# Optimization experiments

Measured on AMD Instinct MI355X. Metric: run time of the kernel, lower is better.

## Reference

```python
import jax, jax.numpy as jnp
import numpy as np

B, M, E, NPOS, F, NHEAD, NLAYERS, DFF = 32, 512, 512, 1024, 768, 8, 2, 2048
S = M + 1

def _pe(embed, pad):
    pos = np.arange(pad, dtype=np.float32)[:, None]
    i = np.arange(embed)[None, :]
    ang = pos / np.power(10000.0, (i // 2 * 2.0) / embed)
    pe = np.where(i % 2 == 0, np.sin(ang), np.cos(ang))
    return jnp.asarray(pe, jnp.float32)

PE = _pe(E, M)  # [M, E] sinusoidal table, matches pos_embedding()

def _ln(x, w, b, eps=1e-5):
    mu = x.mean(-1, keepdims=True)
    var = ((x - mu) ** 2).mean(-1, keepdims=True)
    return (x - mu) / jnp.sqrt(var + eps) * w + b

def _mha(x, wi, bi, wo, bo):
    # x: [L, N, E] where L is the attended axis (torch seq dim)
    L, N, Em = x.shape
    Dh = Em // NHEAD
    q, k, v = jnp.split(x @ wi.T + bi, 3, axis=-1)
    q = q.reshape(L, N, NHEAD, Dh) * np.float32(1.0 / np.sqrt(Dh))
    k = k.reshape(L, N, NHEAD, Dh)
    v = v.reshape(L, N, NHEAD, Dh)
    att = jax.nn.softmax(jnp.einsum('lnhd,mnhd->nhlm', q, k), axis=-1)
    o = jnp.einsum('nhlm,mnhd->lnhd', att, v).reshape(L, N, Em)
    return o @ wo.T + bo

def _encoder(x, enc):
    wi, bi, wo, bo, ln1w, ln1b, ln2w, ln2b, w1, b1, w2, b2 = enc
    for l in range(NLAYERS):  # post-norm TransformerEncoderLayer, ReLU, eval mode
        x = _ln(x + _mha(x, wi[l], bi[l], wo[l], bo[l]), ln1w[l], ln1b[l])
        h = jax.nn.relu(x @ w1[l].T + b1[l]) @ w2[l].T + b2[l]
        x = _ln(x + h, ln2w[l], ln2b[l])
    return x

def _forward(pos1, pos2, bert_feature, final_base, emb_table, enc, w_model, w_disc, b_disc):
    emb_table = emb_table.at[0].set(0.0)  # padding_idx=0
    embed = emb_table[pos2] + PE          # [B, M, E]
    starts, ends = pos1[..., 0], pos1[..., 1]
    # loop breaks at first span with end==0: valid = prefix of nonzero ends
    valid = jnp.cumprod((ends != 0).astype(jnp.int32), axis=1).astype(bool)
    k = jnp.arange(M)
    cover = valid[:, :, None] & (starts[:, :, None] <= k) & (k < ends[:, :, None])  # [B, Mspan, Mpos]
    # later spans overwrite earlier ones -> take max covering span index
    span_id = jnp.max(jnp.where(cover, jnp.arange(M)[None, :, None], -1), axis=1)  # [B, Mpos]
    filled = jnp.take_along_axis(embed, jnp.clip(span_id, 0, M - 1)[..., None], axis=1)
    final = jnp.where(span_id[..., None] >= 0, filled, final_base)  # [B, M, E]
    cls = jnp.broadcast_to(emb_table[1], (B, 1, E))
    x = jnp.concatenate([cls, final], axis=1)  # [B, S, E]; torch encoder treats dim0 as seq
    x = _encoder(x, enc)
    pos_feature = jnp.tanh(x @ w_model.T)      # [B, S, F]
    z = jnp.concatenate([bert_feature, pos_feature], axis=-1) @ w_disc.T + b_disc
    return jax.nn.sigmoid(z)                   # [B, S, 1]

def setup_inputs():
    key = jax.random.key(0)
    ks = jax.random.split(key, 12)
    sc = 0.02
    n_valid, chunk = 120, 4  # contiguous spans [4j, 4j+4) for j < 120, then end==0 terminator
    j = np.arange(M)
    starts = np.where(j < n_valid, j * chunk, 0)
    ends = np.where(j < n_valid, j * chunk + chunk, 0)
    pos1 = np.broadcast_to(np.stack([starts, ends], -1), (B, M, 2)).astype(np.int32)
    return {
        'pos1': jnp.asarray(pos1),
        'pos2': jax.random.randint(ks[0], (B, M), 2, NPOS),
        'bert_feature': jax.random.normal(ks[1], (B, S, F), jnp.float32),
        'final_base': jax.random.uniform(ks[2], (B, M, E), jnp.float32),
        'emb_table': jax.random.normal(ks[3], (NPOS, E), jnp.float32) * sc,
        'enc_in_proj_w': jax.random.normal(ks[4], (NLAYERS, 3 * E, E), jnp.float32) * sc,
        'enc_in_proj_b': jnp.zeros((NLAYERS, 3 * E), jnp.float32),
        'enc_out_proj_w': jax.random.normal(ks[5], (NLAYERS, E, E), jnp.float32) * sc,
        'enc_out_proj_b': jnp.zeros((NLAYERS, E), jnp.float32),
        'enc_ln1_w': jnp.ones((NLAYERS, E), jnp.float32),
        'enc_ln1_b': jnp.zeros((NLAYERS, E), jnp.float32),
        'enc_ln2_w': jnp.ones((NLAYERS, E), jnp.float32),
        'enc_ln2_b': jnp.zeros((NLAYERS, E), jnp.float32),
        'enc_ffn_w1': jax.random.normal(ks[6], (NLAYERS, DFF, E), jnp.float32) * sc,
        'enc_ffn_b1': jnp.zeros((NLAYERS, DFF), jnp.float32),
        'enc_ffn_w2': jax.random.normal(ks[7], (NLAYERS, E, DFF), jnp.float32) * sc,
        'enc_ffn_b2': jnp.zeros((NLAYERS, E), jnp.float32),
        'w_model': jax.random.normal(ks[8], (F, E), jnp.float32) * sc,
        'w_disc': jax.random.normal(ks[9], (1, 2 * F), jnp.float32) * sc,
        'b_disc': jnp.zeros((1,), jnp.float32),
    }

def reference(pos1, pos2, bert_feature, final_base, emb_table,
              enc_in_proj_w, enc_in_proj_b, enc_out_proj_w, enc_out_proj_b,
              enc_ln1_w, enc_ln1_b, enc_ln2_w, enc_ln2_b,
              enc_ffn_w1, enc_ffn_b1, enc_ffn_w2, enc_ffn_b2,
              w_model, w_disc, b_disc):
    enc = (enc_in_proj_w, enc_in_proj_b, enc_out_proj_w, enc_out_proj_b,
           enc_ln1_w, enc_ln1_b, enc_ln2_w, enc_ln2_b,
           enc_ffn_w1, enc_ffn_b1, enc_ffn_w2, enc_ffn_b2)
    return _forward(pos1, pos2, bert_feature, final_base, emb_table, enc, w_model, w_disc, b_disc)
```

## Files before the change

### kernel.cpp

```cpp
#include <hip/hip_runtime.h>
#include <hip/hip_bf16.h>

#define B_   32
#define M_   512
#define E_   512
#define S_   513
#define T_   (B_ * S_)
#define TP_  16512
#define NH_  8
#define DH_  64
#define F_   768
#define DFF_ 2048

#define GMT_ 129

typedef short short8 __attribute__((ext_vector_type(8)));
typedef float floatx4 __attribute__((ext_vector_type(4)));

__device__ __forceinline__ float bf2f(unsigned short u) {
    return __uint_as_float(((unsigned int)u) << 16);
}
__device__ __forceinline__ unsigned short f2b_rne(float f) {
    unsigned int u = __float_as_uint(f);
    unsigned int r = u + 0x7FFF + ((u >> 16) & 1);
    return (unsigned short)(r >> 16);
}
__device__ __forceinline__ void gload16(const void* g, void* l) {
    __builtin_amdgcn_global_load_lds(
        (const __attribute__((address_space(1))) void*)g,
        (__attribute__((address_space(3))) void*)l, 16, 0, 0);
}
__device__ __forceinline__ void wait_vm0() { __builtin_amdgcn_s_waitcnt(0x0F70); }

__global__ void span_kernel(const int* __restrict__ pos1, int* __restrict__ span) {
    int b = blockIdx.x;
    __shared__ int st[M_], en[M_];
    __shared__ int nv;
    int tid = threadIdx.x;
    for (int j = tid; j < M_; j += 256) {
        st[j] = pos1[(b * M_ + j) * 2];
        en[j] = pos1[(b * M_ + j) * 2 + 1];
    }
    __syncthreads();
    if (tid == 0) {
        int n = M_;
        for (int j = 0; j < M_; ++j) if (en[j] == 0) { n = j; break; }
        nv = n;
    }
    __syncthreads();
    int n = nv;
    for (int k = tid; k < M_; k += 256) {
        int best = -1;
        for (int j = 0; j < n; ++j)
            if (st[j] <= k && k < en[j]) best = j;
        span[b * M_ + k] = best;
    }
}

__global__ void f2b5_kernel(const float* __restrict__ s0, const float* __restrict__ s1,
                            const float* __restrict__ s2, const float* __restrict__ s3,
                            const float* __restrict__ s4,
                            unsigned short* __restrict__ dst,
                            int c0, int c1, int c2, int c3, int c4) {
    int i = blockIdx.x * 256 + threadIdx.x;
    if (i >= c4) return;
    float v;
    if      (i < c0) v = s0[i];
    else if (i < c1) v = s1[i - c0];
    else if (i < c2) v = s2[i - c1];
    else if (i < c3) v = s3[i - c2];
    else             v = s4[i - c3];
    dst[i] = f2b_rne(v);
}

__global__ void build_x(const float* __restrict__ emb,
                        const int* __restrict__ pos2,
                        const float* __restrict__ fbase,
                        const int* __restrict__ span,
                        float* __restrict__ x,
                        unsigned short* __restrict__ xb) {
    long long idx = (long long)blockIdx.x * blockDim.x + threadIdx.x;
    if (idx >= (long long)T_ * E_) return;
    int e = (int)(idx % E_);
    int t = (int)(idx / E_);
    int s = t % S_;
    int b = t / S_;
    float val;
    if (s == 0) {
        val = emb[E_ + e];
    } else {
        int k = s - 1;
        int sid = span[b * M_ + k];
        if (sid >= 0) {
            int p = pos2[b * M_ + sid];
            float ex = (float)((e >> 1) << 1) * (1.0f / 512.0f);
            float ang = (float)sid * exp2f(-ex * 13.287712379549449f);
            float pe = (e & 1) ? cosf(ang) : sinf(ang);
            val = emb[(size_t)p * E_ + e] + pe;
        } else {
            val = fbase[((size_t)b * M_ + k) * E_ + e];
        }
    }
    x[idx] = val;
    xb[idx] = f2b_rne(val);
}

template <int ACT, int KT>
__global__ __launch_bounds__(256, 4) void gemm_bf16(const unsigned short* __restrict__ A,
                                                    const unsigned short* __restrict__ W,
                                                    const float* __restrict__ bias,
                                                    unsigned short* __restrict__ Cb,
                                                    int T, int O) {
    constexpr int K = KT;
    constexpr int NSTEP = K / 32;
    __shared__ __align__(16) unsigned short sA[2][128 * 32];
    __shared__ __align__(16) unsigned short sB[2][128 * 32];
    int tid = threadIdx.x;
    int lane = tid & 63, wv = tid >> 6;
    int wr = (wv >> 1) * 64, wc = (wv & 1) * 64;

    int gn = O / 128;
    int per_panel = 8 * gn;
    int id = blockIdx.x;
    int p = id / per_panel;
    int r = id - p * per_panel;
    int mrem = GMT_ - p * 8; if (mrem > 8) mrem = 8;
    int mt = p * 8 + r % mrem;
    int nt = r / mrem;
    int t0 = mt * 128, o0 = nt * 128;

    floatx4 acc[4][4] = {};

    const unsigned short* Ag = A + (size_t)(t0 + wv * 32 + (lane >> 2)) * K + (lane & 3) * 8;
    const unsigned short* Bg = W + (size_t)(o0 + wv * 32 + (lane >> 2)) * K + (lane & 3) * 8;
    const size_t row16 = (size_t)16 * K;
    unsigned short* dA0 = &sA[0][wv * 1024];
    unsigned short* dB0 = &sB[0][wv * 1024];

    int fr = lane & 15;
    int fk = (lane >> 4) * 8;

    gload16(Ag, dA0);
    gload16(Ag + row16, dA0 + 512);
    gload16(Bg, dB0);
    gload16(Bg + row16, dB0 + 512);
    wait_vm0();
    __syncthreads();

#pragma unroll 2
    for (int s = 0; s < NSTEP; ++s) {
        const int cur = s & 1;
        if (s + 1 < NSTEP) {
            const int k = (s + 1) * 32;
            unsigned short* dA = &sA[cur ^ 1][wv * 1024];
            unsigned short* dB = &sB[cur ^ 1][wv * 1024];
            gload16(Ag + k, dA);
            gload16(Ag + row16 + k, dA + 512);
            gload16(Bg + k, dB);
            gload16(Bg + row16 + k, dB + 512);
        }

        short8 af[4], bfr[4];
#pragma unroll
        for (int i = 0; i < 4; ++i)
            af[i] = *(const short8*)&sA[cur][(wr + i * 16 + fr) * 32 + fk];
#pragma unroll
        for (int j = 0; j < 4; ++j)
            bfr[j] = *(const short8*)&sB[cur][(wc + j * 16 + fr) * 32 + fk];
#pragma unroll
        for (int i = 0; i < 4; ++i)
#pragma unroll
            for (int j = 0; j < 4; ++j)
                acc[i][j] = __builtin_amdgcn_mfma_f32_16x16x32_bf16(af[i], bfr[j], acc[i][j], 0, 0, 0);

        wait_vm0();
        __syncthreads();
    }

    int cr = (lane >> 4) * 4;
    int cc = lane & 15;
#pragma unroll
    for (int i = 0; i < 4; ++i) {
#pragma unroll
        for (int j = 0; j < 4; ++j) {
            int gn_ = o0 + wc + j * 16 + cc;
            float bv = bias ? bias[gn_] : 0.f;
#pragma unroll
            for (int rr = 0; rr < 4; ++rr) {
                int gm_ = t0 + wr + i * 16 + cr + rr;
                if (gm_ >= T) continue;
                float v = acc[i][j][rr] + bv;
                if (ACT == 1) v = fmaxf(v, 0.f);
                if (ACT == 2) v = tanhf(v);
                Cb[(size_t)gm_ * O + gn_] = f2b_rne(v);
            }
        }
    }
}

__global__ __launch_bounds__(64) void attn_mfma(const unsigned short* __restrict__ qkv,
                                                unsigned short* __restrict__ o) {
    __shared__ __align__(16) unsigned short vt[64 * 40];
    __shared__ __align__(16) unsigned short ps[32 * 40];
    int s = blockIdx.x, h = blockIdx.y;
    int lane = threadIdx.x;
    int hd = h * 64;
    int fr = lane & 15, fq = lane >> 4;

    {
        int m = lane >> 1;
        int d0 = (lane & 1) * 32;
        const unsigned short* vrow = qkv + ((size_t)m * S_ + s) * 1536 + 1024 + hd + d0;
        short8 v0 = *(const short8*)(vrow);
        short8 v1 = *(const short8*)(vrow + 8);
        short8 v2 = *(const short8*)(vrow + 16);
        short8 v3 = *(const short8*)(vrow + 24);
#pragma unroll
        for (int j = 0; j < 8; ++j) {
            vt[(d0 + j) * 40 + m]      = (unsigned short)v0[j];
            vt[(d0 + 8 + j) * 40 + m]  = (unsigned short)v1[j];
            vt[(d0 + 16 + j) * 40 + m] = (unsigned short)v2[j];
            vt[(d0 + 24 + j) * 40 + m] = (unsigned short)v3[j];
        }
    }

    floatx4 c[2][2] = {};
#pragma unroll
    for (int ks = 0; ks < 2; ++ks) {
        short8 aq[2], bk[2];
#pragma unroll
        for (int lt = 0; lt < 2; ++lt) {
            int l = lt * 16 + fr;
            aq[lt] = *(const short8*)(qkv + ((size_t)l * S_ + s) * 1536 + hd + ks * 32 + fq * 8);
        }
#pragma unroll
        for (int mt = 0; mt < 2; ++mt) {
            int m = mt * 16 + fr;
            bk[mt] = *(const short8*)(qkv + ((size_t)m * S_ + s) * 1536 + 512 + hd + ks * 32 + fq * 8);
        }
#pragma unroll
        for (int lt = 0; lt < 2; ++lt)
#pragma unroll
            for (int mt = 0; mt < 2; ++mt)
                c[lt][mt] = __builtin_amdgcn_mfma_f32_16x16x32_bf16(aq[lt], bk[mt], c[lt][mt], 0, 0, 0);
    }

#pragma unroll
    for (int lt = 0; lt < 2; ++lt) {
#pragma unroll
        for (int r = 0; r < 4; ++r) {
            float a = c[lt][0][r] * 0.125f;
            float b = c[lt][1][r] * 0.125f;
            float mx = fmaxf(a, b);
#pragma unroll
            for (int off = 1; off < 16; off <<= 1) mx = fmaxf(mx, __shfl_xor(mx, off));
            float ea = expf(a - mx), eb = expf(b - mx);
            float sm = ea + eb;
#pragma unroll
            for (int off = 1; off < 16; off <<= 1) sm += __shfl_xor(sm, off);
            float inv = 1.f / sm;
            int l = lt * 16 + fq * 4 + r;
            ps[l * 40 + fr]      = f2b_rne(ea * inv);
            ps[l * 40 + 16 + fr] = f2b_rne(eb * inv);
        }
    }
    __syncthreads();

    short8 pa[2], vb[4];
#pragma unroll
    for (int lt = 0; lt < 2; ++lt)
        pa[lt] = *(const short8*)&ps[(lt * 16 + fr) * 40 + fq * 8];
#pragma unroll
    for (int dt = 0; dt < 4; ++dt)
        vb[dt] = *(const short8*)&vt[(dt * 16 + fr) * 40 + fq * 8];

    floatx4 oa[2][4] = {};
#pragma unroll
    for (int lt = 0; lt < 2; ++lt)
#pragma unroll
        for (int dt = 0; dt < 4; ++dt)
            oa[lt][dt] = __builtin_amdgcn_mfma_f32_16x16x32_bf16(pa[lt], vb[dt], oa[lt][dt], 0, 0, 0);

#pragma unroll
    for (int lt = 0; lt < 2; ++lt)
#pragma unroll
        for (int dt = 0; dt < 4; ++dt)
#pragma unroll
            for (int r = 0; r < 4; ++r) {
                int l = lt * 16 + fq * 4 + r;
                o[((size_t)l * S_ + s) * E_ + hd + dt * 16 + fr] = f2b_rne(oa[lt][dt][r]);
            }
}

__global__ __launch_bounds__(256) void add_ln(float* __restrict__ x,
                                              unsigned short* __restrict__ xb,
                                              const unsigned short* __restrict__ h,
                                              const float* __restrict__ w,
                                              const float* __restrict__ b) {
    int t = blockIdx.x;
    float* xr = x + (size_t)t * E_;
    const unsigned short* hr = h + (size_t)t * E_;
    int i0 = threadIdx.x * 2;
    float2 xv = *(const float2*)&xr[i0];
    ushort2 hv = *(const ushort2*)&hr[i0];
    float v0 = xv.x + bf2f(hv.x), v1 = xv.y + bf2f(hv.y);

    __shared__ float red[4];
    float sum = v0 + v1;
    for (int off = 32; off; off >>= 1) sum += __shfl_down(sum, off);
    if ((threadIdx.x & 63) == 0) red[threadIdx.x >> 6] = sum;
    __syncthreads();
    float mu = (red[0] + red[1] + red[2] + red[3]) * (1.0f / E_);
    __syncthreads();

    float d0 = v0 - mu, d1 = v1 - mu;
    float qs = d0 * d0 + d1 * d1;
    for (int off = 32; off; off >>= 1) qs += __shfl_down(qs, off);
    if ((threadIdx.x & 63) == 0) red[threadIdx.x >> 6] = qs;
    __syncthreads();
    float var = (red[0] + red[1] + red[2] + red[3]) * (1.0f / E_);
    float rstd = rsqrtf(var + 1e-5f);

    float o0 = d0 * rstd * w[i0]     + b[i0];
    float o1 = d1 * rstd * w[i0 + 1] + b[i0 + 1];
    *(float2*)&xr[i0] = make_float2(o0, o1);
    xb[(size_t)t * E_ + i0]     = f2b_rne(o0);
    xb[(size_t)t * E_ + i0 + 1] = f2b_rne(o1);
}

__global__ __launch_bounds__(256) void disc_kernel(const float* __restrict__ bert,
                                                   const unsigned short* __restrict__ pf,
                                                   const float* __restrict__ wd,
                                                   const float* __restrict__ bd,
                                                   float* __restrict__ out) {
    int t = blockIdx.x;
    float s = 0.f;
    for (int f = threadIdx.x; f < F_; f += 256) {
        s += bert[(size_t)t * F_ + f] * wd[f];
        s += bf2f(pf[(size_t)t * F_ + f]) * wd[F_ + f];
    }
    for (int off = 32; off; off >>= 1) s += __shfl_down(s, off);
    __shared__ float red[4];
    if ((threadIdx.x & 63) == 0) red[threadIdx.x >> 6] = s;
    __syncthreads();
    if (threadIdx.x == 0) {
        float z = red[0] + red[1] + red[2] + red[3] + bd[0];
        out[t] = 1.f / (1.f + expf(-z));
    }
}

extern "C" void kernel_launch(void* const* d_in, const int* in_sizes, int n_in,
                              void* d_out, int out_size, void* d_ws, size_t ws_size,
                              hipStream_t stream) {
    const int*   pos1 = (const int*)d_in[0];
    const int*   pos2 = (const int*)d_in[1];
    const float* bert = (const float*)d_in[2];
    const float* fb   = (const float*)d_in[3];
    const float* emb  = (const float*)d_in[4];
    const float* wi   = (const float*)d_in[5];
    const float* bi   = (const float*)d_in[6];
    const float* wo   = (const float*)d_in[7];
    const float* bo   = (const float*)d_in[8];
    const float* ln1w = (const float*)d_in[9];
    const float* ln1b = (const float*)d_in[10];
    const float* ln2w = (const float*)d_in[11];
    const float* ln2b = (const float*)d_in[12];
    const float* w1   = (const float*)d_in[13];
    const float* b1   = (const float*)d_in[14];
    const float* w2   = (const float*)d_in[15];
    const float* b2   = (const float*)d_in[16];
    const float* wm   = (const float*)d_in[17];
    const float* wd   = (const float*)d_in[18];
    const float* bd   = (const float*)d_in[19];
    float* out = (float*)d_out;

    float* ws   = (float*)d_ws;
    int*   span = (int*)ws;
    float* x    = ws + 16384;
    unsigned short* xb  = (unsigned short*)(x + (size_t)T_ * 512);
    unsigned short* atb = xb + (size_t)TP_ * 512;
    unsigned short* hb  = atb + (size_t)TP_ * 512;
    unsigned short* U   = hb + (size_t)T_ * 512;
    unsigned short* qkvb = U;
    unsigned short* h1b  = U;
    unsigned short* pfb  = U;
    unsigned short* wib  = U + (size_t)TP_ * 2048;
    const int NWI = 2 * 1536 * 512;
    const int NWO = 2 * 512 * 512;
    const int NW1 = 2 * 2048 * 512;
    const int NW2 = 2 * 512 * 2048;
    const int NWM = 768 * 512;
    unsigned short* wob = wib + NWI;
    unsigned short* w1b = wob + NWO;
    unsigned short* w2b = w1b + NW1;
    unsigned short* wmb = w2b + NW2;

    span_kernel<<<B_, 256, 0, stream>>>(pos1, span);
    {
        int c0 = NWI, c1 = c0 + NWO, c2 = c1 + NW1, c3 = c2 + NW2, c4 = c3 + NWM;
        f2b5_kernel<<<(c4 + 255) / 256, 256, 0, stream>>>(wi, wo, w1, w2, wm, wib,
                                                          c0, c1, c2, c3, c4);
    }
    build_x<<<(int)(((long long)T_ * 512 + 255) / 256), 256, 0, stream>>>(emb, pos2, fb, span, x, xb);

    for (int l = 0; l < 2; ++l) {
        gemm_bf16<0, 512><<<GMT_ * (1536 / 128), 256, 0, stream>>>(
            xb, wib + (size_t)l * 1536 * 512, bi + l * 1536, qkvb, T_, 1536);
        attn_mfma<<<dim3(S_, NH_), 64, 0, stream>>>(qkvb, atb);
        gemm_bf16<0, 512><<<GMT_ * (512 / 128), 256, 0, stream>>>(
            atb, wob + (size_t)l * 512 * 512, bo + l * 512, hb, T_, 512);
        add_ln<<<T_, 256, 0, stream>>>(x, xb, hb, ln1w + l * 512, ln1b + l * 512);
        gemm_bf16<1, 512><<<GMT_ * (2048 / 128), 256, 0, stream>>>(
            xb, w1b + (size_t)l * 2048 * 512, b1 + l * 2048, h1b, T_, 2048);
        gemm_bf16<0, 2048><<<GMT_ * (512 / 128), 256, 0, stream>>>(
            h1b, w2b + (size_t)l * 512 * 2048, b2 + l * 512, hb, T_, 512);
        add_ln<<<T_, 256, 0, stream>>>(x, xb, hb, ln2w + l * 512, ln2b + l * 512);
    }
    gemm_bf16<2, 512><<<GMT_ * (768 / 128), 256, 0, stream>>>(
        xb, wmb, nullptr, pfb, T_, 768);
    disc_kernel<<<T_, 256, 0, stream>>>(bert, pfb, wd, bd, out);
}
```

Measured before the change: 777.1 us.

## Triple-buffer GEMM LDS pipeline and vectorize weight bf16 conversion

The bf16 GEMM moves from double to triple buffering in LDS. Global-to-LDS loads are issued two K-steps ahead, and a partial vmcnt wait lets the newest loads stay in flight while the current tile is computed. This hides more memory latency per block, at the cost of 50% more shared memory and a lower occupancy target in launch bounds (3 blocks instead of 4). The weight fp32-to-bf16 conversion kernel now handles four elements per thread with float4 loads and ushort4 stores.

Result: slower. 805.7 us (+3.7%).

```diff
diff --git a/kernel.cpp b/kernel.cpp
--- a/kernel.cpp
+++ b/kernel.cpp
@@ -31,6 +31,7 @@
         (__attribute__((address_space(3))) void*)l, 16, 0, 0);
 }
 __device__ __forceinline__ void wait_vm0() { __builtin_amdgcn_s_waitcnt(0x0F70); }
+__device__ __forceinline__ void wait_vm4() { __builtin_amdgcn_s_waitcnt(0x0F74); }
 
 __global__ void span_kernel(const int* __restrict__ pos1, int* __restrict__ span) {
     int b = blockIdx.x;
@@ -62,15 +63,19 @@
                             const float* __restrict__ s4,
                             unsigned short* __restrict__ dst,
                             int c0, int c1, int c2, int c3, int c4) {
-    int i = blockIdx.x * 256 + threadIdx.x;
+    int i = (blockIdx.x * 256 + threadIdx.x) * 4;
     if (i >= c4) return;
-    float v;
-    if      (i < c0) v = s0[i];
-    else if (i < c1) v = s1[i - c0];
-    else if (i < c2) v = s2[i - c1];
-    else if (i < c3) v = s3[i - c2];
-    else             v = s4[i - c3];
-    dst[i] = f2b_rne(v);
+    const float* src; int off;
+    if      (i < c0) { src = s0; off = i; }
+    else if (i < c1) { src = s1; off = i - c0; }
+    else if (i < c2) { src = s2; off = i - c1; }
+    else if (i < c3) { src = s3; off = i - c2; }
+    else             { src = s4; off = i - c3; }
+    float4 v = *(const float4*)(src + off);
+    ushort4 o;
+    o.x = f2b_rne(v.x); o.y = f2b_rne(v.y);
+    o.z = f2b_rne(v.z); o.w = f2b_rne(v.w);
+    *(ushort4*)(dst + i) = o;
 }
 
 __global__ void build_x(const float* __restrict__ emb,
@@ -106,15 +111,15 @@
 }
 
 template <int ACT, int KT>
-__global__ __launch_bounds__(256, 4) void gemm_bf16(const unsigned short* __restrict__ A,
+__global__ __launch_bounds__(256, 3) void gemm_bf16(const unsigned short* __restrict__ A,
                                                     const unsigned short* __restrict__ W,
                                                     const float* __restrict__ bias,
                                                     unsigned short* __restrict__ Cb,
                                                     int T, int O) {
     constexpr int K = KT;
     constexpr int NSTEP = K / 32;
-    __shared__ __align__(16) unsigned short sA[2][128 * 32];
-    __shared__ __align__(16) unsigned short sB[2][128 * 32];
+    __shared__ __align__(16) unsigned short sA[3][128 * 32];
+    __shared__ __align__(16) unsigned short sB[3][128 * 32];
     int tid = threadIdx.x;
     int lane = tid & 63, wv = tid >> 6;
     int wr = (wv >> 1) * 64, wc = (wv & 1) * 64;
@@ -134,26 +139,36 @@
     const unsigned short* Ag = A + (size_t)(t0 + wv * 32 + (lane >> 2)) * K + (lane & 3) * 8;
     const unsigned short* Bg = W + (size_t)(o0 + wv * 32 + (lane >> 2)) * K + (lane & 3) * 8;
     const size_t row16 = (size_t)16 * K;
-    unsigned short* dA0 = &sA[0][wv * 1024];
-    unsigned short* dB0 = &sB[0][wv * 1024];
-
     int fr = lane & 15;
     int fk = (lane >> 4) * 8;
 
-    gload16(Ag, dA0);
-    gload16(Ag + row16, dA0 + 512);
-    gload16(Bg, dB0);
-    gload16(Bg + row16, dB0 + 512);
-    wait_vm0();
-    __syncthreads();
-
-#pragma unroll 2
+    {
+        unsigned short* dA = &sA[0][wv * 1024];
+        unsigned short* dB = &sB[0][wv * 1024];
+        gload16(Ag, dA);
+        gload16(Ag + row16, dA + 512);
+        gload16(Bg, dB);
+        gload16(Bg + row16, dB + 512);
+    }
+    {
+        unsigned short* dA = &sA[1][wv * 1024];
+        unsigned short* dB = &sB[1][wv * 1024];
+        gload16(Ag + 32, dA);
+        gload16(Ag + row16 + 32, dA + 512);
+        gload16(Bg + 32, dB);
+        gload16(Bg + row16 + 32, dB + 512);
+    }
+
+    int cur = 0, nx2 = 2;
     for (int s = 0; s < NSTEP; ++s) {
-        const int cur = s & 1;
-        if (s + 1 < NSTEP) {
-            const int k = (s + 1) * 32;
-            unsigned short* dA = &sA[cur ^ 1][wv * 1024];
-            unsigned short* dB = &sB[cur ^ 1][wv * 1024];
+        if (s < NSTEP - 1) wait_vm4();
+        else               wait_vm0();
+        __syncthreads();
+
+        if (s + 2 < NSTEP) {
+            const int k = (s + 2) * 32;
+            unsigned short* dA = &sA[nx2][wv * 1024];
+            unsigned short* dB = &sB[nx2][wv * 1024];
             gload16(Ag + k, dA);
             gload16(Ag + row16 + k, dA + 512);
             gload16(Bg + k, dB);
@@ -173,8 +188,8 @@
             for (int j = 0; j < 4; ++j)
                 acc[i][j] = __builtin_amdgcn_mfma_f32_16x16x32_bf16(af[i], bfr[j], acc[i][j], 0, 0, 0);
 
-        wait_vm0();
-        __syncthreads();
+        cur = (cur == 2) ? 0 : cur + 1;
+        nx2 = (nx2 == 2) ? 0 : nx2 + 1;
     }
 
     int cr = (lane >> 4) * 4;
@@ -398,8 +413,8 @@
     span_kernel<<<B_, 256, 0, stream>>>(pos1, span);
     {
         int c0 = NWI, c1 = c0 + NWO, c2 = c1 + NW1, c3 = c2 + NW2, c4 = c3 + NWM;
-        f2b5_kernel<<<(c4 + 255) / 256, 256, 0, stream>>>(wi, wo, w1, w2, wm, wib,
-                                                          c0, c1, c2, c3, c4);
+        f2b5_kernel<<<(c4 / 4 + 255) / 256, 256, 0, stream>>>(wi, wo, w1, w2, wm, wib,
+                                                              c0, c1, c2, c3, c4);
     }
     build_x<<<(int)(((long long)T_ * 512 + 255) / 256), 256, 0, stream>>>(emb, pos2, fb, span, x, xb);
 
```
